# Optimization experiments

Hardware: AMD Instinct MI355X
Metric: run time of the kernel (lower is better)

Reference implementation:

```python
import jax, jax.numpy as jnp
import numpy as np

L, K, HID, OUT, B, N, E = 2, 3, 64, 32, 8, 10000, 160000


def setup_inputs() -> dict:
    key = jax.random.key(0)
    ks = jax.random.split(key, 12)
    s = 0.05
    return {
        "edge_weight": jax.random.uniform(ks[1], (E,), dtype=jnp.float32),
        "hidden_states": jax.random.normal(ks[2], (L, B, N, HID), dtype=jnp.float32),
        "go_input": jax.random.normal(ks[3], (B, N, HID), dtype=jnp.float32),
        "Wz": jax.random.normal(ks[4], (L, 2, K, 2 * HID, HID), dtype=jnp.float32) * s,
        "bz": jnp.zeros((L, HID), dtype=jnp.float32),
        "Wr": jax.random.normal(ks[5], (L, 2, K, 2 * HID, HID), dtype=jnp.float32) * s,
        "br": jnp.zeros((L, HID), dtype=jnp.float32),
        "Wh": jax.random.normal(ks[6], (L, 2, K, 2 * HID, HID), dtype=jnp.float32) * s,
        "bh": jnp.zeros((L, HID), dtype=jnp.float32),
        "proj_W": jax.random.normal(ks[7], (HID, OUT), dtype=jnp.float32) * s,
        "proj_b": jnp.zeros((OUT,), dtype=jnp.float32),
        "edge_index": jax.random.randint(ks[0], (2, E), 0, N, dtype=jnp.int32),
    }


def _prop(z, s_idx, d_idx, nw):
    # z: [B,N,F]; aggregate nw-weighted source features at destinations
    m = z[:, s_idx, :] * nw[None, :, None]  # [B,E,F]
    return jnp.zeros_like(z).at[:, d_idx, :].add(m)


def _dconv(x, W, b, src, dst, norm_out, norm_in):
    # x: [B,N,Fin]; W: [2,K,Fin,Fout] (dir 0 = forward walk, dir 1 = reverse)
    H = jnp.einsum('bnf,fo->bno', x, W[0, 0] + W[1, 0])  # T0 shared
    To_pp, Ti_pp = x, x
    To_p = _prop(x, src, dst, norm_out)
    Ti_p = _prop(x, dst, src, norm_in)
    H = H + jnp.einsum('bnf,fo->bno', To_p, W[0, 1]) + jnp.einsum('bnf,fo->bno', Ti_p, W[1, 1])
    for k in range(2, K):  # Chebyshev recursion over hops
        To = 2.0 * _prop(To_p, src, dst, norm_out) - To_pp
        Ti = 2.0 * _prop(Ti_p, dst, src, norm_in) - Ti_pp
        H = H + jnp.einsum('bnf,fo->bno', To, W[0, k]) + jnp.einsum('bnf,fo->bno', Ti, W[1, k])
        To_pp, To_p = To_p, To
        Ti_pp, Ti_p = Ti_p, Ti
    return H + b


def _cell(x, h, Wz, bz, Wr, br, Wh, bh, src, dst, no, ni):
    xh = jnp.concatenate([x, h], axis=-1)
    Z = jax.nn.sigmoid(_dconv(xh, Wz, bz, src, dst, no, ni))
    R = jax.nn.sigmoid(_dconv(xh, Wr, br, src, dst, no, ni))
    Ht = jnp.tanh(_dconv(jnp.concatenate([x, R * h], axis=-1), Wh, bh, src, dst, no, ni))
    return Z * h + (1.0 - Z) * Ht


def reference(edge_weight, hidden_states, go_input, Wz, bz, Wr, br, Wh, bh, proj_W, proj_b, edge_index):
    src, dst = edge_index[0], edge_index[1]
    deg_out = jax.ops.segment_sum(edge_weight, src, num_segments=N)
    deg_in = jax.ops.segment_sum(edge_weight, dst, num_segments=N)
    inv_out = 1.0 / jnp.where(deg_out > 0, deg_out, 1.0)
    inv_in = 1.0 / jnp.where(deg_in > 0, deg_in, 1.0)
    norm_out = edge_weight * inv_out[src]
    norm_in = edge_weight * inv_in[dst]

    cur = go_input
    last = cur
    for l in range(L):  # small fixed layer loop (dropout=0 -> identity)
        last = _cell(cur, hidden_states[l], Wz[l], bz[l], Wr[l], br[l], Wh[l], bh[l],
                     src, dst, norm_out, norm_in)
        if l < L - 1:
            cur = last
    return jnp.einsum('bnh,ho->bno', last, proj_W) + proj_b
```

## Files before the change

### kernel.cpp

```cpp
#include <hip/hip_runtime.h>
#include <math.h>

#define NL 2
#define KK 3
#define HIDD 64
#define OUTD 32
#define NB 8
#define NN 10000
#define NE 160000
#define ROWS 80000
#define WSTRIDE (128*HIDD)

typedef __attribute__((ext_vector_type(8))) short bf16x8;
typedef __attribute__((ext_vector_type(8))) unsigned short u16x8;
typedef __attribute__((ext_vector_type(4))) unsigned short u16x4;
typedef __attribute__((ext_vector_type(4))) float f32x4;

__device__ __forceinline__ ushort f2b(float x) {
    union { float f; unsigned u; } v; v.f = x;
    unsigned r = (v.u + 0x7fff + ((v.u >> 16) & 1)) >> 16;
    return (ushort)r;
}
__device__ __forceinline__ float b2f(ushort u) {
    union { unsigned u; float f; } v; v.u = (unsigned)u << 16;
    return v.f;
}

__global__ void zero_kernel(int* p, long n) {
    long t = (long)blockIdx.x * blockDim.x + threadIdx.x;
    if (t < n) p[t] = 0;
}

__global__ void deg_cnt_kernel(const float* __restrict__ w, const int* __restrict__ src,
                               const int* __restrict__ dst, float* deg_out, float* deg_in,
                               int* cnt_f, int* cnt_r) {
    int e = blockIdx.x * blockDim.x + threadIdx.x;
    if (e >= NE) return;
    int s = src[e], d = dst[e];
    float we = w[e];
    atomicAdd(&deg_out[s], we);
    atomicAdd(&deg_in[d], we);
    atomicAdd(&cnt_f[d], 1);
    atomicAdd(&cnt_r[s], 1);
}

__global__ void scan_kernel(const int* __restrict__ cnt, int* __restrict__ off) {
    __shared__ int part[256];
    const int CH = (NN + 255) / 256;
    int t = threadIdx.x;
    int s = 0;
    for (int i = 0; i < CH; ++i) {
        int idx = t * CH + i;
        if (idx < NN) s += cnt[idx];
    }
    part[t] = s;
    __syncthreads();
    if (t == 0) {
        int run = 0;
        for (int i = 0; i < 256; ++i) { int v = part[i]; part[i] = run; run += v; }
        off[NN] = run;
    }
    __syncthreads();
    int run = part[t];
    for (int i = 0; i < CH; ++i) {
        int idx = t * CH + i;
        if (idx < NN) { off[idx] = run; run += cnt[idx]; }
    }
}

__global__ void copy_pos_kernel(const int* __restrict__ off_f, const int* __restrict__ off_r,
                                int* pos_f, int* pos_r) {
    int t = blockIdx.x * blockDim.x + threadIdx.x;
    if (t < NN) { pos_f[t] = off_f[t]; pos_r[t] = off_r[t]; }
}

__global__ void fill_kernel(const float* __restrict__ w, const int* __restrict__ src,
                            const int* __restrict__ dst, const float* __restrict__ deg_out,
                            const float* __restrict__ deg_in,
                            int* pos_f, int* pos_r,
                            int* col_f, float* w_f, int* col_r, float* w_r) {
    int e = blockIdx.x * blockDim.x + threadIdx.x;
    if (e >= NE) return;
    int s = src[e], d = dst[e];
    float we = w[e];
    float dgo = deg_out[s]; dgo = (dgo > 0.f) ? dgo : 1.f;
    float dgi = deg_in[d];  dgi = (dgi > 0.f) ? dgi : 1.f;
    int pf = atomicAdd(&pos_f[d], 1);
    col_f[pf] = s; w_f[pf] = we / dgo;
    int pr = atomicAdd(&pos_r[s], 1);
    col_r[pr] = d; w_r[pr] = we / dgi;
}

__global__ void convW_kernel(const float* __restrict__ Wz, const float* __restrict__ Wr,
                             const float* __restrict__ Wh, ushort* __restrict__ Wt) {
    int t = blockIdx.x * 256 + threadIdx.x;
    if (t >= 2 * 3 * 2 * 3 * 64 * 128) return;
    int f = t & 127;
    int r1 = t >> 7;
    int o = r1 & 63;
    int r2 = r1 >> 6;
    int k = r2 % 3;
    int r3 = r2 / 3;
    int d = r3 & 1;
    int r4 = r3 >> 1;
    int g = r4 % 3;
    int l = r4 / 3;
    const float* W = (g == 0) ? Wz : (g == 1) ? Wr : Wh;
    float v = W[(((long)(l * 2 + d) * 3 + k) * 128 + f) * 64 + o];
    if (k == 0 && d == 0)
        v += W[(((long)(l * 2 + 1) * 3 + 0) * 128 + f) * 64 + o];
    Wt[t] = f2b(v);
}

__global__ void convX_perm(const float* __restrict__ in, ushort* __restrict__ xh, int c,
                           float* __restrict__ hp) {
    long t = (long)blockIdx.x * blockDim.x + threadIdx.x;
    if (t >= (long)ROWS * 16) return;
    int q = (int)(t & 15);
    long rowin = t >> 4;
    int b = (int)(rowin / NN);
    int n = (int)(rowin - (long)b * NN);
    f32x4 v = __builtin_nontemporal_load((const f32x4*)&in[t * 4]);
    u16x4 r;
    r.x = f2b(v.x); r.y = f2b(v.y); r.z = f2b(v.z); r.w = f2b(v.w);
    long orow = (long)n * 8 + b;
    *(u16x4*)&xh[orow * 128 + c * 64 + q * 4] = r;
    if (hp) *(f32x4*)&hp[orow * 64 + q * 4] = v;
}

struct PropCfg {
    const ushort* X[2];
    const ushort* base[2];
    const int*    off[2];
    const int*    col[2];
    const float*  w[2];
    ushort*       out[2];
};

template<int HALF, int NDIR>
__global__ __launch_bounds__(128) void prop_slice(PropCfg C, float alpha, float beta) {
    constexpr int LPG = HALF ? 8 : 16;
    constexpr int GPB = 128 / LPG;
    int bid = blockIdx.x;
    int b = bid & 7;
    int r = bid >> 3;
    int dir, tile;
    if (NDIR == 2) { dir = r & 1; tile = r >> 1; }
    else           { dir = 0;     tile = r; }
    int g    = threadIdx.x / LPG;
    int lane = threadIdx.x % LPG;
    int n = tile * GPB + g;
    const ushort* X   = C.X[dir];
    const ushort* bas = C.base[dir];
    const int*    off = C.off[dir];
    const int*    col = C.col[dir];
    const float*  w   = C.w[dir];
    ushort*       out = C.out[dir];
    int s = off[n], e = off[n + 1];
    int eo = b * 128 + (HALF ? 64 : 0) + lane * 8;
    float acc[8];
    #pragma unroll
    for (int i = 0; i < 8; ++i) acc[i] = 0.f;
    int j = s;
    for (; j + 2 <= e; j += 2) {
        int c0 = col[j], c1 = col[j + 1];
        float w0 = w[j], w1 = w[j + 1];
        u16x8 v0 = *(const u16x8*)&X[(long)c0 * 1024 + eo];
        u16x8 v1 = *(const u16x8*)&X[(long)c1 * 1024 + eo];
        #pragma unroll
        for (int i = 0; i < 8; ++i) acc[i] = fmaf(b2f(v0[i]), w0, acc[i]);
        #pragma unroll
        for (int i = 0; i < 8; ++i) acc[i] = fmaf(b2f(v1[i]), w1, acc[i]);
    }
    if (j < e) {
        int c = col[j];
        float ww = w[j];
        u16x8 v = *(const u16x8*)&X[(long)c * 1024 + eo];
        #pragma unroll
        for (int i = 0; i < 8; ++i) acc[i] = fmaf(b2f(v[i]), ww, acc[i]);
    }
    long o = (long)n * 1024 + eo;
    #pragma unroll
    for (int i = 0; i < 8; ++i) acc[i] *= alpha;
    if (beta != 0.f) {
        u16x8 bb = *(const u16x8*)&bas[o];
        #pragma unroll
        for (int i = 0; i < 8; ++i) acc[i] = fmaf(beta, b2f(bb[i]), acc[i]);
    }
    u16x8 rr;
    #pragma unroll
    for (int i = 0; i < 8; ++i) rr[i] = f2b(acc[i]);
    *(u16x8*)&out[o] = rr;
}

struct GM {
    const ushort* X[10];
    const ushort* Wa[10];
    const ushort* Wb[10];
};

#define LOADF4(tt, aa, bb)                                                         \
    {                                                                              \
        const ushort* Xp = A.X[tt];                                                \
        const ushort* Wp = gate ? A.Wb[tt] : A.Wa[tt];                             \
        _Pragma("unroll")                                                          \
        for (int ks = 0; ks < 2; ++ks) {                                           \
            _Pragma("unroll")                                                      \
            for (int mi = 0; mi < 4; ++mi)                                         \
                aa[ks][mi] = *(const bf16x8*)&Xp[(grow + mi * 16 + lr) * 128 +     \
                                                 ks * 32 + lk * 8];                \
            _Pragma("unroll")                                                      \
            for (int ni = 0; ni < 4; ++ni)                                         \
                bb[ks][ni] = *(const bf16x8*)&Wp[(ni * 16 + lr) * 128 +            \
                                                 ks * 32 + lk * 8];                \
        }                                                                          \
    }

#define MFMAF4(aa, bb)                                                             \
    _Pragma("unroll")                                                              \
    for (int ks = 0; ks < 2; ++ks)                                                 \
        _Pragma("unroll")                                                          \
        for (int mi = 0; mi < 4; ++mi)                                             \
            _Pragma("unroll")                                                      \
            for (int ni = 0; ni < 4; ++ni)                                         \
                acc[mi][ni] = __builtin_amdgcn_mfma_f32_16x16x32_bf16(             \
                    aa[ks][mi], bb[ks][ni], acc[mi][ni], 0, 0, 0);

template<int NT>
__global__ __launch_bounds__(256, 2) void mfma_dual(GM A,
        const float* __restrict__ bzp, const float* __restrict__ brp,
        const float* __restrict__ hp,
        float* __restrict__ Z, ushort* __restrict__ xh) {
    int lane = threadIdx.x & 63;
    int wid  = threadIdx.x >> 6;
    int gate = wid >> 1;
    long grow = (long)blockIdx.x * 128 + (long)(wid & 1) * 64;
    int lr = lane & 15;
    int lk = lane >> 4;
    f32x4 acc[4][4];
    #pragma unroll
    for (int i = 0; i < 4; ++i)
        #pragma unroll
        for (int j = 0; j < 4; ++j)
            acc[i][j] = (f32x4){0.f, 0.f, 0.f, 0.f};

    bf16x8 a0[2][4], b0[2][4], a1[2][4], b1[2][4];
    LOADF4(0, a0, b0);
    #pragma unroll
    for (int tt = 0; tt < NT; tt += 2) {
        if (tt + 1 < NT) LOADF4(tt + 1, a1, b1);
        MFMAF4(a0, b0);
        if (tt + 2 < NT) LOADF4(tt + 2, a0, b0);
        if (tt + 1 < NT) MFMAF4(a1, b1);
    }

    const float* bias = gate ? brp : bzp;
    #pragma unroll
    for (int mi = 0; mi < 4; ++mi) {
        #pragma unroll
        for (int q = 0; q < 4; ++q) {
            long row = grow + mi * 16 + lk * 4 + q;
            #pragma unroll
            for (int ni = 0; ni < 4; ++ni) {
                int colc = ni * 16 + lr;
                float v = acc[mi][ni][q] + bias[colc];
                float sg = 1.f / (1.f + expf(-v));
                if (gate == 0) {
                    Z[row * 64 + colc] = sg;
                } else {
                    float hv = hp[row * 64 + colc];
                    xh[row * 128 + 64 + colc] = f2b(sg * hv);
                }
            }
        }
    }
}

template<int NT>
__global__ __launch_bounds__(128, 2) void mfma_single(GM A,
        const float* __restrict__ bhp, const float* __restrict__ hp,
        const float* __restrict__ Zg,
        float* __restrict__ outF, ushort* __restrict__ xh, int writeF) {
    int lane = threadIdx.x & 63;
    int wid  = threadIdx.x >> 6;
    const int gate = 0;
    long grow = (long)blockIdx.x * 128 + (long)wid * 64;
    int lr = lane & 15;
    int lk = lane >> 4;
    f32x4 acc[4][4];
    #pragma unroll
    for (int i = 0; i < 4; ++i)
        #pragma unroll
        for (int j = 0; j < 4; ++j)
            acc[i][j] = (f32x4){0.f, 0.f, 0.f, 0.f};

    bf16x8 a0[2][4], b0[2][4], a1[2][4], b1[2][4];
    LOADF4(0, a0, b0);
    #pragma unroll
    for (int tt = 0; tt < NT; tt += 2) {
        if (tt + 1 < NT) LOADF4(tt + 1, a1, b1);
        MFMAF4(a0, b0);
        if (tt + 2 < NT) LOADF4(tt + 2, a0, b0);
        if (tt + 1 < NT) MFMAF4(a1, b1);
    }

    #pragma unroll
    for (int mi = 0; mi < 4; ++mi) {
        #pragma unroll
        for (int q = 0; q < 4; ++q) {
            long row = grow + mi * 16 + lk * 4 + q;
            #pragma unroll
            for (int ni = 0; ni < 4; ++ni) {
                int colc = ni * 16 + lr;
                float v = acc[mi][ni][q] + bhp[colc];
                float ht = tanhf(v);
                float z = Zg[row * 64 + colc];
                float hv = hp[row * 64 + colc];
                float res = z * hv + (1.f - z) * ht;
                if (writeF) outF[row * 64 + colc] = res;
                else        xh[row * 128 + colc] = f2b(res);
            }
        }
    }
}

__global__ void proj_kernel(const float* __restrict__ last, const float* __restrict__ W,
                            const float* __restrict__ bias, float* __restrict__ out) {
    long t = (long)blockIdx.x * blockDim.x + threadIdx.x;
    if (t >= (long)ROWS * OUTD) return;
    long row = t >> 5;
    int  o   = (int)(t & 31);
    int n = (int)(row >> 3), b = (int)(row & 7);
    float acc = bias[o];
    #pragma unroll
    for (int hh = 0; hh < HIDD; ++hh)
        acc = fmaf(last[row * 64 + hh], W[hh * OUTD + o], acc);
    out[((long)b * NN + n) * 32 + o] = acc;
}

extern "C" void kernel_launch(void* const* d_in, const int* in_sizes, int n_in,
                              void* d_out, int out_size, void* d_ws, size_t ws_size,
                              hipStream_t stream) {
    const float* edge_weight = (const float*)d_in[0];
    const float* hidden      = (const float*)d_in[1];
    const float* go_input    = (const float*)d_in[2];
    const float* Wz = (const float*)d_in[3];
    const float* bz = (const float*)d_in[4];
    const float* Wr = (const float*)d_in[5];
    const float* br = (const float*)d_in[6];
    const float* Wh = (const float*)d_in[7];
    const float* bh = (const float*)d_in[8];
    const float* projW = (const float*)d_in[9];
    const float* projb = (const float*)d_in[10];
    const int*   eidx  = (const int*)d_in[11];
    const int* src = eidx;
    const int* dst = eidx + NE;
    float* out = (float*)d_out;

    char* p = (char*)d_ws;
    auto alloc = [&](size_t bytes) { char* r = p; p += (bytes + 15) & ~(size_t)15; return r; };
    float* deg_out = (float*)alloc(NN * 4);
    float* deg_in  = (float*)alloc(NN * 4);
    int*   cnt_f   = (int*)alloc(NN * 4);
    int*   cnt_r   = (int*)alloc(NN * 4);
    int*   off_f   = (int*)alloc((NN + 4) * 4);
    int*   off_r   = (int*)alloc((NN + 4) * 4);
    int*   pos_f   = (int*)alloc(NN * 4);
    int*   pos_r   = (int*)alloc(NN * 4);
    int*   col_f   = (int*)alloc(NE * 4);
    float* w_f     = (float*)alloc(NE * 4);
    int*   col_r   = (int*)alloc(NE * 4);
    float* w_r     = (float*)alloc(NE * 4);
    ushort* Wt     = (ushort*)alloc((size_t)2 * 3 * 2 * 3 * 64 * 128 * 2);
    const size_t XB = (size_t)ROWS * 128 * 2;
    ushort* xh  = (ushort*)alloc(XB);
    ushort* Tf1 = (ushort*)alloc(XB);
    ushort* Tf2 = (ushort*)alloc(XB);
    ushort* Tr1 = (ushort*)alloc(XB);
    ushort* Tr2 = (ushort*)alloc(XB);
    float*  Zbuf = (float*)alloc((size_t)ROWS * HIDD * 4);
    float*  hp   = (float*)alloc((size_t)ROWS * HIDD * 4);
    if ((size_t)(p - (char*)d_ws) > ws_size) return;

    const int TB = 256;
    const int EGRID = (NE + TB - 1) / TB;
    const int NGRID = (NN + TB - 1) / TB;

    zero_kernel<<<(4 * NN + TB - 1) / TB, TB, 0, stream>>>((int*)deg_out, 4 * NN);
    deg_cnt_kernel<<<EGRID, TB, 0, stream>>>(edge_weight, src, dst, deg_out, deg_in, cnt_f, cnt_r);
    scan_kernel<<<1, 256, 0, stream>>>(cnt_f, off_f);
    scan_kernel<<<1, 256, 0, stream>>>(cnt_r, off_r);
    copy_pos_kernel<<<NGRID, TB, 0, stream>>>(off_f, off_r, pos_f, pos_r);
    fill_kernel<<<EGRID, TB, 0, stream>>>(edge_weight, src, dst, deg_out, deg_in,
                                          pos_f, pos_r, col_f, w_f, col_r, w_r);

    convW_kernel<<<2304, 256, 0, stream>>>(Wz, Wr, Wh, Wt);
    convX_perm<<<5000, 256, 0, stream>>>(go_input, xh, 0, nullptr);

    auto wt_term = [&](int l, int g, int d, int k, int c) -> const ushort* {
        return Wt + ((((long)((l * 3 + g) * 2 + d) * 3 + k) * 64) * 128) + (long)c * 64;
    };
    const int dd[5]  = {0, 0, 0, 1, 1};
    const int kk2[5] = {0, 1, 2, 1, 2};

    for (int l = 0; l < NL; ++l) {
        const float* h = hidden + (long)l * ROWS * HIDD;
        convX_perm<<<5000, 256, 0, stream>>>(h, xh, 1, hp);

        {
            PropCfg c1{};
            c1.X[0] = xh;  c1.off[0] = off_f; c1.col[0] = col_f; c1.w[0] = w_f; c1.out[0] = Tf1;
            c1.X[1] = xh;  c1.off[1] = off_r; c1.col[1] = col_r; c1.w[1] = w_r; c1.out[1] = Tr1;
            prop_slice<0, 2><<<(NN / 8) * 2 * 8, 128, 0, stream>>>(c1, 1.f, 0.f);
            PropCfg c2f{};
            c2f.X[0] = Tf1; c2f.base[0] = xh;
            c2f.off[0] = off_f; c2f.col[0] = col_f; c2f.w[0] = w_f; c2f.out[0] = Tf2;
            prop_slice<0, 1><<<(NN / 8) * 8, 128, 0, stream>>>(c2f, 2.f, -1.f);
            PropCfg c2r{};
            c2r.X[0] = Tr1; c2r.base[0] = xh;
            c2r.off[0] = off_r; c2r.col[0] = col_r; c2r.w[0] = w_r; c2r.out[0] = Tr2;
            prop_slice<0, 1><<<(NN / 8) * 8, 128, 0, stream>>>(c2r, 2.f, -1.f);
        }

        const ushort* xs[5] = {xh, Tf1, Tf2, Tr1, Tr2};
        GM A{};
        for (int i = 0; i < 5; ++i) {
            A.X[i]      = xs[i];
            A.X[5 + i]  = xs[i] + 64;
            A.Wa[i]     = wt_term(l, 0, dd[i], kk2[i], 0);
            A.Wa[5 + i] = wt_term(l, 0, dd[i], kk2[i], 1);
            A.Wb[i]     = wt_term(l, 1, dd[i], kk2[i], 0);
            A.Wb[5 + i] = wt_term(l, 1, dd[i], kk2[i], 1);
        }
        mfma_dual<10><<<ROWS / 128, 256, 0, stream>>>(A, bz + l * HIDD, br + l * HIDD,
                                                      hp, Zbuf, xh);

        {
            PropCfg c1{};
            c1.X[0] = xh;  c1.off[0] = off_f; c1.col[0] = col_f; c1.w[0] = w_f; c1.out[0] = Tf1;
            c1.X[1] = xh;  c1.off[1] = off_r; c1.col[1] = col_r; c1.w[1] = w_r; c1.out[1] = Tr1;
            prop_slice<1, 2><<<(NN / 16) * 2 * 8, 128, 0, stream>>>(c1, 1.f, 0.f);
            PropCfg c2{};
            c2.X[0] = Tf1; c2.base[0] = xh;
            c2.off[0] = off_f; c2.col[0] = col_f; c2.w[0] = w_f; c2.out[0] = Tf2;
            c2.X[1] = Tr1; c2.base[1] = xh;
            c2.off[1] = off_r; c2.col[1] = col_r; c2.w[1] = w_r; c2.out[1] = Tr2;
            prop_slice<1, 2><<<(NN / 16) * 2 * 8, 128, 0, stream>>>(c2, 2.f, -1.f);
        }

        GM Ah{};
        for (int i = 0; i < 5; ++i) {
            Ah.X[i]      = xs[i];
            Ah.X[5 + i]  = xs[i] + 64;
            Ah.Wa[i]     = wt_term(l, 2, dd[i], kk2[i], 0);
            Ah.Wa[5 + i] = wt_term(l, 2, dd[i], kk2[i], 1);
        }
        mfma_single<10><<<ROWS / 128, 128, 0, stream>>>(Ah, bh + l * HIDD, hp, Zbuf,
                                                        Zbuf, xh, (l == NL - 1) ? 1 : 0);
    }

    proj_kernel<<<(int)(((long)ROWS * OUTD + TB - 1) / TB), TB, 0, stream>>>(
        Zbuf, projW, projb, out);
}
```

Baseline: 970.9 us.

## Stage activation tiles in swizzled LDS with double buffering for MFMA gate kernels

Replaces the two MFMA gate kernels, which loaded activation fragments straight from global memory into registers, with one templated kernel. It stages each 128-row activation tile cooperatively into shared memory, uses an XOR swizzle to avoid bank conflicts, and double-buffers across the five terms with a barrier per step. The candidate kernel now runs 256 threads with each wave owning 32 rows instead of 64, which doubles the waves per tile. The aim is coalesced global loads and sharing one tile between the z and r gate waves, at the cost of 64KB of LDS per block, which may limit occupancy.

Result: no change. 988.4 us (+1.8%).

```diff
diff --git a/kernel.cpp b/kernel.cpp
--- a/kernel.cpp
+++ b/kernel.cpp
@@ -193,132 +193,129 @@
     *(u16x8*)&out[o] = rr;
 }
 
-struct GM {
-    const ushort* X[10];
+struct GM5 {
+    const ushort* Xb[5];
     const ushort* Wa[10];
     const ushort* Wb[10];
 };
 
-#define LOADF4(tt, aa, bb)                                                         \
-    {                                                                              \
-        const ushort* Xp = A.X[tt];                                                \
-        const ushort* Wp = gate ? A.Wb[tt] : A.Wa[tt];                             \
-        _Pragma("unroll")                                                          \
-        for (int ks = 0; ks < 2; ++ks) {                                           \
-            _Pragma("unroll")                                                      \
-            for (int mi = 0; mi < 4; ++mi)                                         \
-                aa[ks][mi] = *(const bf16x8*)&Xp[(grow + mi * 16 + lr) * 128 +     \
-                                                 ks * 32 + lk * 8];                \
-            _Pragma("unroll")                                                      \
-            for (int ni = 0; ni < 4; ++ni)                                         \
-                bb[ks][ni] = *(const bf16x8*)&Wp[(ni * 16 + lr) * 128 +            \
-                                                 ks * 32 + lk * 8];                \
-        }                                                                          \
-    }
-
-#define MFMAF4(aa, bb)                                                             \
-    _Pragma("unroll")                                                              \
-    for (int ks = 0; ks < 2; ++ks)                                                 \
-        _Pragma("unroll")                                                          \
-        for (int mi = 0; mi < 4; ++mi)                                             \
-            _Pragma("unroll")                                                      \
-            for (int ni = 0; ni < 4; ++ni)                                         \
-                acc[mi][ni] = __builtin_amdgcn_mfma_f32_16x16x32_bf16(             \
-                    aa[ks][mi], bb[ks][ni], acc[mi][ni], 0, 0, 0);
-
-template<int NT>
-__global__ __launch_bounds__(256, 2) void mfma_dual(GM A,
-        const float* __restrict__ bzp, const float* __restrict__ brp,
-        const float* __restrict__ hp,
-        float* __restrict__ Z, ushort* __restrict__ xh) {
-    int lane = threadIdx.x & 63;
-    int wid  = threadIdx.x >> 6;
-    int gate = wid >> 1;
-    long grow = (long)blockIdx.x * 128 + (long)(wid & 1) * 64;
+template<int DUAL>
+__global__ __launch_bounds__(256, 2) void mfma_lds(GM5 A,
+        const float* __restrict__ bias0, const float* __restrict__ bias1,
+        const float* __restrict__ hp, float* __restrict__ Z,
+        ushort* __restrict__ xh, const float* __restrict__ Zg,
+        float* __restrict__ outF, int writeF) {
+    constexpr int MI = DUAL ? 4 : 2;
+    __shared__ ushort sx[2][16384];
+    int tid  = threadIdx.x;
+    int lane = tid & 63;
+    int wid  = tid >> 6;
     int lr = lane & 15;
     int lk = lane >> 4;
-    f32x4 acc[4][4];
-    #pragma unroll
-    for (int i = 0; i < 4; ++i)
+    int gate  = DUAL ? (wid >> 1) : 0;
+    int wrow0 = DUAL ? ((wid & 1) * 64) : (wid * 32);
+
+    f32x4 acc[MI][4];
+    #pragma unroll
+    for (int i = 0; i < MI; ++i)
         #pragma unroll
         for (int j = 0; j < 4; ++j)
             acc[i][j] = (f32x4){0.f, 0.f, 0.f, 0.f};
 
-    bf16x8 a0[2][4], b0[2][4], a1[2][4], b1[2][4];
-    LOADF4(0, a0, b0);
-    #pragma unroll
-    for (int tt = 0; tt < NT; tt += 2) {
-        if (tt + 1 < NT) LOADF4(tt + 1, a1, b1);
-        MFMAF4(a0, b0);
-        if (tt + 2 < NT) LOADF4(tt + 2, a0, b0);
-        if (tt + 1 < NT) MFMAF4(a1, b1);
-    }
-
-    const float* bias = gate ? brp : bzp;
-    #pragma unroll
-    for (int mi = 0; mi < 4; ++mi) {
-        #pragma unroll
-        for (int q = 0; q < 4; ++q) {
-            long row = grow + mi * 16 + lk * 4 + q;
+    u16x8 streg[8];
+    auto load_tile = [&](int t) {
+        const u16x8* g = (const u16x8*)(A.Xb[t] + (size_t)blockIdx.x * 16384);
+        #pragma unroll
+        for (int k = 0; k < 8; ++k) streg[k] = g[tid + k * 256];
+    };
+    auto write_tile = [&](int bi) {
+        #pragma unroll
+        for (int k = 0; k < 8; ++k) {
+            int unit = tid + k * 256;
+            int row = unit >> 4, c16 = unit & 15;
+            int u2 = (row << 4) | (c16 ^ (row & 7));
+            *(u16x8*)&sx[bi][u2 << 3] = streg[k];
+        }
+    };
+
+    load_tile(0);
+    write_tile(0);
+    __syncthreads();
+
+    int cur = 0;
+    #pragma unroll
+    for (int t = 0; t < 5; ++t) {
+        if (t < 4) load_tile(t + 1);
+        #pragma unroll
+        for (int c = 0; c < 2; ++c) {
+            const ushort* Wp = DUAL ? (gate ? A.Wb[c * 5 + t] : A.Wa[c * 5 + t])
+                                    : A.Wa[c * 5 + t];
+            bf16x8 b[2][4];
             #pragma unroll
-            for (int ni = 0; ni < 4; ++ni) {
-                int colc = ni * 16 + lr;
-                float v = acc[mi][ni][q] + bias[colc];
-                float sg = 1.f / (1.f + expf(-v));
-                if (gate == 0) {
-                    Z[row * 64 + colc] = sg;
-                } else {
-                    float hv = hp[row * 64 + colc];
-                    xh[row * 128 + 64 + colc] = f2b(sg * hv);
+            for (int ks = 0; ks < 2; ++ks)
+                #pragma unroll
+                for (int ni = 0; ni < 4; ++ni)
+                    b[ks][ni] = *(const bf16x8*)&Wp[(ni * 16 + lr) * 128 +
+                                                    ks * 32 + lk * 8];
+            #pragma unroll
+            for (int ks = 0; ks < 2; ++ks)
+                #pragma unroll
+                for (int mi = 0; mi < MI; ++mi) {
+                    int r = wrow0 + mi * 16 + lr;
+                    int c16 = (c << 3) | (ks << 2) | lk;
+                    bf16x8 av = *(const bf16x8*)&sx[cur][(r << 7) +
+                                                         ((c16 ^ (r & 7)) << 3)];
+                    #pragma unroll
+                    for (int ni = 0; ni < 4; ++ni)
+                        acc[mi][ni] = __builtin_amdgcn_mfma_f32_16x16x32_bf16(
+                            av, b[ks][ni], acc[mi][ni], 0, 0, 0);
+                }
+        }
+        if (t < 4) {
+            write_tile(cur ^ 1);
+            __syncthreads();
+            cur ^= 1;
+        }
+    }
+
+    if (DUAL) {
+        const float* bias = gate ? bias1 : bias0;
+        #pragma unroll
+        for (int mi = 0; mi < MI; ++mi) {
+            #pragma unroll
+            for (int q = 0; q < 4; ++q) {
+                long row = (long)blockIdx.x * 128 + wrow0 + mi * 16 + lk * 4 + q;
+                #pragma unroll
+                for (int ni = 0; ni < 4; ++ni) {
+                    int colc = ni * 16 + lr;
+                    float v = acc[mi][ni][q] + bias[colc];
+                    float sg = 1.f / (1.f + expf(-v));
+                    if (gate == 0) {
+                        Z[row * 64 + colc] = sg;
+                    } else {
+                        float hv = hp[row * 64 + colc];
+                        xh[row * 128 + 64 + colc] = f2b(sg * hv);
+                    }
                 }
             }
         }
-    }
-}
-
-template<int NT>
-__global__ __launch_bounds__(128, 2) void mfma_single(GM A,
-        const float* __restrict__ bhp, const float* __restrict__ hp,
-        const float* __restrict__ Zg,
-        float* __restrict__ outF, ushort* __restrict__ xh, int writeF) {
-    int lane = threadIdx.x & 63;
-    int wid  = threadIdx.x >> 6;
-    const int gate = 0;
-    long grow = (long)blockIdx.x * 128 + (long)wid * 64;
-    int lr = lane & 15;
-    int lk = lane >> 4;
-    f32x4 acc[4][4];
-    #pragma unroll
-    for (int i = 0; i < 4; ++i)
-        #pragma unroll
-        for (int j = 0; j < 4; ++j)
-            acc[i][j] = (f32x4){0.f, 0.f, 0.f, 0.f};
-
-    bf16x8 a0[2][4], b0[2][4], a1[2][4], b1[2][4];
-    LOADF4(0, a0, b0);
-    #pragma unroll
-    for (int tt = 0; tt < NT; tt += 2) {
-        if (tt + 1 < NT) LOADF4(tt + 1, a1, b1);
-        MFMAF4(a0, b0);
-        if (tt + 2 < NT) LOADF4(tt + 2, a0, b0);
-        if (tt + 1 < NT) MFMAF4(a1, b1);
-    }
-
-    #pragma unroll
-    for (int mi = 0; mi < 4; ++mi) {
-        #pragma unroll
-        for (int q = 0; q < 4; ++q) {
-            long row = grow + mi * 16 + lk * 4 + q;
+    } else {
+        #pragma unroll
+        for (int mi = 0; mi < MI; ++mi) {
             #pragma unroll
-            for (int ni = 0; ni < 4; ++ni) {
-                int colc = ni * 16 + lr;
-                float v = acc[mi][ni][q] + bhp[colc];
-                float ht = tanhf(v);
-                float z = Zg[row * 64 + colc];
-                float hv = hp[row * 64 + colc];
-                float res = z * hv + (1.f - z) * ht;
-                if (writeF) outF[row * 64 + colc] = res;
-                else        xh[row * 128 + colc] = f2b(res);
+            for (int q = 0; q < 4; ++q) {
+                long row = (long)blockIdx.x * 128 + wrow0 + mi * 16 + lk * 4 + q;
+                #pragma unroll
+                for (int ni = 0; ni < 4; ++ni) {
+                    int colc = ni * 16 + lr;
+                    float v = acc[mi][ni][q] + bias0[colc];
+                    float ht = tanhf(v);
+                    float z = Zg[row * 64 + colc];
+                    float hv = hp[row * 64 + colc];
+                    float res = z * hv + (1.f - z) * ht;
+                    if (writeF) outF[row * 64 + colc] = res;
+                    else        xh[row * 128 + colc] = f2b(res);
+                }
             }
         }
     }
@@ -423,17 +420,16 @@
         }
 
         const ushort* xs[5] = {xh, Tf1, Tf2, Tr1, Tr2};
-        GM A{};
+        GM5 A{};
         for (int i = 0; i < 5; ++i) {
-            A.X[i]      = xs[i];
-            A.X[5 + i]  = xs[i] + 64;
+            A.Xb[i] = xs[i];
             A.Wa[i]     = wt_term(l, 0, dd[i], kk2[i], 0);
             A.Wa[5 + i] = wt_term(l, 0, dd[i], kk2[i], 1);
             A.Wb[i]     = wt_term(l, 1, dd[i], kk2[i], 0);
             A.Wb[5 + i] = wt_term(l, 1, dd[i], kk2[i], 1);
         }
-        mfma_dual<10><<<ROWS / 128, 256, 0, stream>>>(A, bz + l * HIDD, br + l * HIDD,
-                                                      hp, Zbuf, xh);
+        mfma_lds<1><<<ROWS / 128, 256, 0, stream>>>(A, bz + l * HIDD, br + l * HIDD,
+                                                    hp, Zbuf, xh, nullptr, nullptr, 0);
 
         {
             PropCfg c1{};
@@ -448,15 +444,15 @@
             prop_slice<1, 2><<<(NN / 16) * 2 * 8, 128, 0, stream>>>(c2, 2.f, -1.f);
         }
 
-        GM Ah{};
+        GM5 Ah{};
         for (int i = 0; i < 5; ++i) {
-            Ah.X[i]      = xs[i];
-            Ah.X[5 + i]  = xs[i] + 64;
+            Ah.Xb[i] = xs[i];
             Ah.Wa[i]     = wt_term(l, 2, dd[i], kk2[i], 0);
             Ah.Wa[5 + i] = wt_term(l, 2, dd[i], kk2[i], 1);
         }
-        mfma_single<10><<<ROWS / 128, 128, 0, stream>>>(Ah, bh + l * HIDD, hp, Zbuf,
-                                                        Zbuf, xh, (l == NL - 1) ? 1 : 0);
+        mfma_lds<0><<<ROWS / 128, 256, 0, stream>>>(Ah, bh + l * HIDD, nullptr,
+                                                    hp, nullptr, xh, Zbuf, Zbuf,
+                                                    (l == NL - 1) ? 1 : 0);
     }
 
     proj_kernel<<<(int)(((long)ROWS * OUTD + TB - 1) / TB), TB, 0, stream>>>(
```
